# Kernel tuning notes

Hardware: AMD Instinct MI355X
Metric: run time of the kernel (lower is better)

## Reference

```python
import jax, jax.numpy as jnp
import numpy as np

B, S, T = 2, 1024, 1024          # batch, new tokens, cache length (prefill: S == T)
DIM, NH, NKV, HD = 2048, 16, 4, 128
FFN = 5632
EPS = 1e-5
STD = 0.02


def rms_norm(x, w, eps=EPS):
    return x * jax.lax.rsqrt(jnp.mean(x * x, axis=-1, keepdims=True) + eps) * w


def apply_rope(x, freqs_cis):
    # x: [B, S, H, HD]; freqs_cis: [S, HD//2, 2] (cos, sin) over consecutive pairs
    xr = x.reshape(*x.shape[:-1], HD // 2, 2)
    cos = freqs_cis[None, :, None, :, 0]
    sin = freqs_cis[None, :, None, :, 1]
    x0, x1 = xr[..., 0], xr[..., 1]
    rot = jnp.stack([x0 * cos - x1 * sin, x0 * sin + x1 * cos], axis=-1)
    return rot.reshape(x.shape)


def setup_inputs() -> dict:
    key = jax.random.key(0)
    ks = jax.random.split(key, 10)
    x = jax.random.normal(ks[0], (B, S, DIM), jnp.float32)
    # rotary tables
    inv_freq = 1.0 / (10000.0 ** (np.arange(0, HD, 2, dtype=np.float32) / HD))
    ang = np.outer(np.arange(S, dtype=np.float32), inv_freq)          # [S, HD//2]
    freqs_cis = jnp.asarray(np.stack([np.cos(ang), np.sin(ang)], -1), jnp.float32)
    cache_k = jnp.zeros((1, B, T, NKV, HD), jnp.float32)
    cache_v = jnp.zeros((1, B, T, NKV, HD), jnp.float32)
    mask = jnp.triu(jnp.full((S, T), -1e9, jnp.float32), k=1)         # additive causal
    wq = jax.random.normal(ks[1], (DIM, NH, HD), jnp.float32) * STD
    wk = jax.random.normal(ks[2], (DIM, NKV, HD), jnp.float32) * STD
    wv = jax.random.normal(ks[3], (DIM, NKV, HD), jnp.float32) * STD
    wo = jax.random.normal(ks[4], (NH * HD, DIM), jnp.float32) * STD
    w_gate = jax.random.normal(ks[5], (DIM, FFN), jnp.float32) * STD
    w_up = jax.random.normal(ks[6], (DIM, FFN), jnp.float32) * STD
    w_down = jax.random.normal(ks[7], (FFN, DIM), jnp.float32) * STD
    attn_norm_w = jnp.ones((DIM,), jnp.float32)
    ffn_norm_w = jnp.ones((DIM,), jnp.float32)
    return dict(x=x, freqs_cis=freqs_cis, cache_k=cache_k, cache_v=cache_v,
                mask=mask, wq=wq, wk=wk, wv=wv, wo=wo, w_gate=w_gate,
                w_up=w_up, w_down=w_down, attn_norm_w=attn_norm_w,
                ffn_norm_w=ffn_norm_w, layer_idx=0)


def reference(x, freqs_cis, cache_k, cache_v, mask, wq, wk, wv, wo,
              w_gate, w_up, w_down, attn_norm_w, ffn_norm_w, layer_idx):
    # --- attention sub-block ---
    h = rms_norm(x, attn_norm_w)
    q = jnp.einsum('bsd,dhk->bshk', h, wq)          # [B,S,NH,HD]
    k = jnp.einsum('bsd,dgk->bsgk', h, wk)          # [B,S,NKV,HD]
    v = jnp.einsum('bsd,dgk->bsgk', h, wv)
    q = apply_rope(q, freqs_cis)
    k = apply_rope(k, freqs_cis)
    # append to per-layer KV cache at position 0 (prefill)
    cache_k = jax.lax.dynamic_update_slice(cache_k, k[None], (layer_idx, 0, 0, 0, 0))
    cache_v = jax.lax.dynamic_update_slice(cache_v, v[None], (layer_idx, 0, 0, 0, 0))
    keys = cache_k[layer_idx]                        # [B,T,NKV,HD]
    vals = cache_v[layer_idx]
    J = NH // NKV                                    # query heads per kv head
    qg = q.reshape(B, S, NKV, J, HD)
    scale = 1.0 / jnp.sqrt(jnp.float32(HD))
    scores = jnp.einsum('bsgjd,btgd->bgjst', qg, keys) * scale  # [B,NKV,J,S,T]
    scores = scores + mask                           # broadcast [S,T]
    probs = jax.nn.softmax(scores, axis=-1)
    ctx = jnp.einsum('bgjst,btgd->bsgjd', probs, vals).reshape(B, S, NH * HD)
    x = x + ctx @ wo
    # --- SwiGLU FFN sub-block ---
    hf = rms_norm(x, ffn_norm_w)
    ffn = (jax.nn.silu(hf @ w_gate) * (hf @ w_up)) @ w_down
    x = x + ffn
    return (x, cache_k, cache_v)
```

## Files before the change

kernel.cpp:

```cpp
#include <hip/hip_runtime.h>

typedef float f32x4 __attribute__((ext_vector_type(4)));
typedef __bf16 bf16x8 __attribute__((ext_vector_type(8)));
typedef unsigned short u16;

#define DIM 2048
#define SEQ 1024
#define BSZ 2
#define NH 16
#define NKV 4
#define HD 128
#define FFNDIM 5632
#define MROWS (BSZ * SEQ)

__device__ __forceinline__ u16 f2bf(float f) {
  union { float f; unsigned u; } v; v.f = f;
  unsigned u = v.u;
  unsigned r = (u + 0x7fffu + ((u >> 16) & 1u)) >> 16;
  return (u16)r;
}
__device__ __forceinline__ float bf2f(u16 h) {
  union { unsigned u; float f; } v; v.u = ((unsigned)h) << 16; return v.f;
}

__device__ __forceinline__ void gld16(const void* g, void* l) {
  __builtin_amdgcn_global_load_lds(
      (const __attribute__((address_space(1))) unsigned int*)g,
      (__attribute__((address_space(3))) unsigned int*)l, 16, 0, 0);
}

__global__ __launch_bounds__(256) void kxpose(const float* __restrict__ W,
                                              u16* __restrict__ Wt,
                                              int K, int N, int rs, int ro) {
  __shared__ float t[64][65];
  int kb = blockIdx.y * 64, nb = blockIdx.x * 64;
  int tid = threadIdx.x;
#pragma unroll
  for (int it = 0; it < 16; ++it) {
    int idx = it * 256 + tid;
    int r = idx >> 6, c = idx & 63;
    t[r][c] = W[(size_t)(kb + r) * N + nb + c];
  }
  __syncthreads();
#pragma unroll
  for (int it = 0; it < 16; ++it) {
    int idx = it * 256 + tid;
    int rn = idx >> 6, ck = idx & 63;
    Wt[((size_t)(nb + rn) * rs + ro) * K + kb + ck] = f2bf(t[ck][rn]);
  }
}

__global__ __launch_bounds__(256) void kvxpose(const u16* __restrict__ v,
                                               u16* __restrict__ vt) {
  __shared__ u16 t[64][66];
  int bg = blockIdx.z;
  int b = bg >> 2, g = bg & 3;
  int s0 = blockIdx.x * 64, d0 = blockIdx.y * 64;
  int tid = threadIdx.x;
  int rr = tid >> 4, cc = (tid & 15) * 4;
#pragma unroll
  for (int it = 0; it < 4; ++it) {
    int r = it * 16 + rr;
    *(uint2*)&t[r][cc] =
        *(const uint2*)(v + (size_t)(b * SEQ + s0 + r) * (NKV * HD) + g * HD + d0 + cc);
  }
  __syncthreads();
#pragma unroll
  for (int it = 0; it < 4; ++it) {
    int r = it * 16 + rr;
    u16 o[4] = {t[cc][r], t[cc + 1][r], t[cc + 2][r], t[cc + 3][r]};
    *(uint2*)(vt + (size_t)((b * NKV + g) * HD + d0 + r) * SEQ + s0 + cc) = *(const uint2*)o;
  }
}

__global__ __launch_bounds__(256) void krmsnorm(const float* __restrict__ x,
                                                const float* __restrict__ w,
                                                u16* __restrict__ out) {
  int row = blockIdx.x, tid = threadIdx.x;
  const float* xr = x + (size_t)row * DIM;
  float4 a = *(const float4*)(xr + tid * 8);
  float4 b = *(const float4*)(xr + tid * 8 + 4);
  float ss = a.x * a.x + a.y * a.y + a.z * a.z + a.w * a.w +
             b.x * b.x + b.y * b.y + b.z * b.z + b.w * b.w;
#pragma unroll
  for (int off = 1; off < 64; off <<= 1) ss += __shfl_xor(ss, off, 64);
  __shared__ float red[4];
  if ((tid & 63) == 0) red[tid >> 6] = ss;
  __syncthreads();
  float tot = red[0] + red[1] + red[2] + red[3];
  float sc = rsqrtf(tot * (1.0f / DIM) + 1e-5f);
  float xs[8] = {a.x, a.y, a.z, a.w, b.x, b.y, b.z, b.w};
  const float* wr = w + tid * 8;
  u16 o[8];
#pragma unroll
  for (int j = 0; j < 8; ++j) o[j] = f2bf(xs[j] * sc * wr[j]);
  *(int4*)(out + (size_t)row * DIM + tid * 8) = *(const int4*)o;
}

__global__ __launch_bounds__(256) void krope_q(u16* __restrict__ q,
                                               const float* __restrict__ fc) {
  int t = blockIdx.x * 256 + threadIdx.x;
  int j = t & 63;
  int h = (t >> 6) & (NH - 1);
  int row = t >> 10;
  int s = row & (SEQ - 1);
  size_t off = (size_t)row * DIM + h * HD + 2 * j;
  unsigned pk = *(unsigned*)(q + off);
  float x0 = bf2f((u16)pk), x1 = bf2f((u16)(pk >> 16));
  float cs = fc[s * HD + 2 * j], sn = fc[s * HD + 2 * j + 1];
  float y0 = x0 * cs - x1 * sn;
  float y1 = x0 * sn + x1 * cs;
  *(unsigned*)(q + off) = (unsigned)f2bf(y0) | ((unsigned)f2bf(y1) << 16);
}

__global__ __launch_bounds__(256) void krope_k(u16* __restrict__ k,
                                               const float* __restrict__ fc,
                                               float* __restrict__ ck) {
  int t = blockIdx.x * 256 + threadIdx.x;
  int j = t & 63;
  int g = (t >> 6) & (NKV - 1);
  int row = t >> 8;
  int s = row & (SEQ - 1);
  size_t off = (size_t)row * (NKV * HD) + g * HD + 2 * j;
  unsigned pk = *(unsigned*)(k + off);
  float x0 = bf2f((u16)pk), x1 = bf2f((u16)(pk >> 16));
  float cs = fc[s * HD + 2 * j], sn = fc[s * HD + 2 * j + 1];
  float y0 = x0 * cs - x1 * sn;
  float y1 = x0 * sn + x1 * cs;
  *(unsigned*)(k + off) = (unsigned)f2bf(y0) | ((unsigned)f2bf(y1) << 16);
  ck[off] = y0;
  ck[off + 1] = y1;
}

template <int EPI>
__global__ __launch_bounds__(512, 4) void kgemm(
    const u16* __restrict__ A, const u16* __restrict__ Bt, int N, int K,
    u16* o0, u16* __restrict__ o1, u16* __restrict__ o2,
    float* of, const float* res) {
  __shared__ u16 As[2][128 * 64];
  __shared__ u16 Bs[2][128 * 64];
  int bn = blockIdx.x * 128, bm = blockIdx.y * 128;
  int tid = threadIdx.x, lane = tid & 63, wv = tid >> 6;
  int wm = (wv >> 2) * 64;
  int wn = (wv & 3) * 32;
  int r16 = lane & 15, grp = lane >> 4;
  int srow = lane >> 3;
  int schunk = ((lane & 7) ^ srow) * 8;
  f32x4 acc[4][2] = {};
  const u16* Abase = A + (size_t)(bm + wv * 16) * K + schunk;
  const u16* Bbase = Bt + (size_t)(bn + wv * 16) * K + schunk;
  int woff = wv * 16 * 64;

  auto STAGE = [&](int buf, int k0) {
#pragma unroll
    for (int j = 0; j < 2; ++j) {
      gld16(Abase + (size_t)(j * 8 + srow) * K + k0, &As[buf][woff + j * 512]);
      gld16(Bbase + (size_t)(j * 8 + srow) * K + k0, &Bs[buf][woff + j * 512]);
    }
  };
  auto COMPUTE = [&](int buf) {
#pragma unroll
    for (int kk = 0; kk < 2; ++kk) {
      int swz = (((kk << 2) | grp) ^ (r16 & 7)) * 8;
      bf16x8 af[4], bfr[2];
#pragma unroll
      for (int m = 0; m < 4; ++m)
        af[m] = *(const bf16x8*)&As[buf][(wm + m * 16 + r16) * 64 + swz];
#pragma unroll
      for (int n = 0; n < 2; ++n)
        bfr[n] = *(const bf16x8*)&Bs[buf][(wn + n * 16 + r16) * 64 + swz];
#pragma unroll
      for (int m = 0; m < 4; ++m)
#pragma unroll
        for (int n = 0; n < 2; ++n)
          acc[m][n] = __builtin_amdgcn_mfma_f32_16x16x32_bf16(af[m], bfr[n], acc[m][n], 0, 0, 0);
    }
  };

  STAGE(0, 0);
  int nt = K >> 6;
  for (int t = 0; t < nt; ++t) {
    int cur = t & 1;
    if (t + 1 < nt) {
      STAGE(cur ^ 1, (t + 1) << 6);
      asm volatile("s_waitcnt vmcnt(4)" ::: "memory");
    } else {
      asm volatile("s_waitcnt vmcnt(0)" ::: "memory");
    }
    __builtin_amdgcn_sched_barrier(0);
    __builtin_amdgcn_s_barrier();
    __builtin_amdgcn_sched_barrier(0);
    COMPUTE(cur);
    __builtin_amdgcn_s_barrier();
  }

#pragma unroll
  for (int mi = 0; mi < 4; ++mi) {
#pragma unroll
    for (int ni = 0; ni < 2; ++ni) {
#pragma unroll
      for (int r = 0; r < 4; ++r) {
        int gr = bm + wm + mi * 16 + grp * 4 + r;
        int gc = bn + wn + ni * 16 + r16;
        float v = acc[mi][ni][r];
        if constexpr (EPI == 0) {
          if (gc < DIM) {
            o0[(size_t)gr * DIM + gc] = f2bf(v);
          } else if (gc < DIM + 512) {
            o1[(size_t)gr * 512 + (gc - DIM)] = f2bf(v);
          } else {
            int c2 = gc - (DIM + 512);
            of[(size_t)gr * 512 + c2] = v;
            o2[(size_t)gr * 512 + c2] = f2bf(v);
          }
        } else {
          of[(size_t)gr * N + gc] = v + res[(size_t)gr * N + gc];
        }
      }
    }
  }
}

__global__ __launch_bounds__(512, 4) void kgemm_gu(
    const u16* __restrict__ A, const u16* __restrict__ Bt,
    u16* __restrict__ out) {
  const int K = DIM;
  __shared__ u16 As[2][128 * 64];
  __shared__ u16 Bs[2][128 * 64];
  int bn = blockIdx.x * 128, bm = blockIdx.y * 128;
  int tid = threadIdx.x, lane = tid & 63, wv = tid >> 6;
  int wm = (wv >> 2) * 64;
  int wn = (wv & 3) * 32;
  int r16 = lane & 15, grp = lane >> 4;
  int srow = lane >> 3;
  int schunk = ((lane & 7) ^ srow) * 8;
  f32x4 acc[4][2] = {};
  const u16* Abase = A + (size_t)(bm + wv * 16) * K + schunk;
  const u16* Bbase = Bt + (size_t)(bn + wv * 16) * K + schunk;
  int woff = wv * 16 * 64;

  auto STAGE = [&](int buf, int k0) {
#pragma unroll
    for (int j = 0; j < 2; ++j) {
      gld16(Abase + (size_t)(j * 8 + srow) * K + k0, &As[buf][woff + j * 512]);
      gld16(Bbase + (size_t)(j * 8 + srow) * K + k0, &Bs[buf][woff + j * 512]);
    }
  };
  auto COMPUTE = [&](int buf) {
#pragma unroll
    for (int kk = 0; kk < 2; ++kk) {
      int swz = (((kk << 2) | grp) ^ (r16 & 7)) * 8;
      bf16x8 af[4], bfr[2];
#pragma unroll
      for (int m = 0; m < 4; ++m)
        af[m] = *(const bf16x8*)&As[buf][(wm + m * 16 + r16) * 64 + swz];
#pragma unroll
      for (int n = 0; n < 2; ++n)
        bfr[n] = *(const bf16x8*)&Bs[buf][(wn + n * 16 + r16) * 64 + swz];
#pragma unroll
      for (int m = 0; m < 4; ++m)
#pragma unroll
        for (int n = 0; n < 2; ++n)
          acc[m][n] = __builtin_amdgcn_mfma_f32_16x16x32_bf16(af[m], bfr[n], acc[m][n], 0, 0, 0);
    }
  };

  STAGE(0, 0);
  int nt = K >> 6;
  for (int t = 0; t < nt; ++t) {
    int cur = t & 1;
    if (t + 1 < nt) {
      STAGE(cur ^ 1, (t + 1) << 6);
      asm volatile("s_waitcnt vmcnt(4)" ::: "memory");
    } else {
      asm volatile("s_waitcnt vmcnt(0)" ::: "memory");
    }
    __builtin_amdgcn_sched_barrier(0);
    __builtin_amdgcn_s_barrier();
    __builtin_amdgcn_sched_barrier(0);
    COMPUTE(cur);
    __builtin_amdgcn_s_barrier();
  }

  bool evenlane = (r16 & 1) == 0;
#pragma unroll
  for (int mi = 0; mi < 4; ++mi) {
#pragma unroll
    for (int ni = 0; ni < 2; ++ni) {
#pragma unroll
      for (int r = 0; r < 4; ++r) {
        float v = acc[mi][ni][r];
        float pv = __shfl_xor(v, 1, 64);
        if (evenlane) {
          int gr = bm + wm + mi * 16 + grp * 4 + r;
          int gc = bn + wn + ni * 16 + r16;
          float sg = v / (1.0f + __expf(-v));
          out[(size_t)gr * FFNDIM + (gc >> 1)] = f2bf(sg * pv);
        }
      }
    }
  }
}

__global__ __launch_bounds__(64) void kattn(const u16* __restrict__ qb,
                                            const u16* __restrict__ kb,
                                            const u16* __restrict__ vtb,
                                            u16* __restrict__ ctxb) {
  __shared__ u16 Plds[16][72];
  int l = threadIdx.x;
  int qt = gridDim.x - 1 - blockIdx.x;
  int h = blockIdx.y, b = blockIdx.z;
  int g = h >> 2;
  int q0 = qt * 16;
  int r16 = l & 15, grp = l >> 4;
  const float scale = 0.08838834764831845f;
  bf16x8 qf[4];
  {
    const u16* qrow = qb + (size_t)(b * SEQ + q0 + r16) * DIM + h * HD + grp * 8;
#pragma unroll
    for (int c = 0; c < 4; ++c) qf[c] = *(const bf16x8*)(qrow + c * 32);
  }
  const u16* vt = vtb + (size_t)(b * NKV + g) * HD * SEQ;
  f32x4 ctx[8] = {};
  float m = -1e30f, lsum = 0.0f;
  int q_idx = q0 + r16;
  int ttmax = (q0 + 15) >> 6;
  for (int tt = 0; tt <= ttmax; ++tt) {
    int t0 = tt * 64;
    f32x4 d[4] = {{0.f, 0.f, 0.f, 0.f}, {0.f, 0.f, 0.f, 0.f},
                  {0.f, 0.f, 0.f, 0.f}, {0.f, 0.f, 0.f, 0.f}};
    const u16* kbase = kb + (size_t)(b * SEQ + t0 + r16) * (NKV * HD) + g * HD + grp * 8;
    __builtin_amdgcn_s_setprio(1);
#pragma unroll
    for (int c = 0; c < 4; ++c) {
#pragma unroll
      for (int ch = 0; ch < 4; ++ch) {
        bf16x8 kf = *(const bf16x8*)(kbase + (size_t)(ch * 16) * (NKV * HD) + c * 32);
        d[ch] = __builtin_amdgcn_mfma_f32_16x16x32_bf16(kf, qf[c], d[ch], 0, 0, 0);
      }
    }
    __builtin_amdgcn_s_setprio(0);
    float p[16];
    float mx = -1e30f;
#pragma unroll
    for (int ch = 0; ch < 4; ++ch) {
#pragma unroll
      for (int r = 0; r < 4; ++r) {
        int tA = t0 + ch * 16 + grp * 4 + r;
        float s = d[ch][r] * scale;
        if (tA > q_idx) s = -1e30f;
        p[ch * 4 + r] = s;
        mx = fmaxf(mx, s);
      }
    }
    mx = fmaxf(mx, __shfl_xor(mx, 16, 64));
    mx = fmaxf(mx, __shfl_xor(mx, 32, 64));
    if (!__all(mx - m <= 8.0f)) {
      float mnew = fmaxf(m, mx);
      float corr = __expf(m - mnew);
      lsum *= corr;
      float cf[4];
#pragma unroll
      for (int r = 0; r < 4; ++r) cf[r] = __shfl(corr, grp * 4 + r, 64);
#pragma unroll
      for (int dc = 0; dc < 8; ++dc)
#pragma unroll
        for (int r = 0; r < 4; ++r) ctx[dc][r] *= cf[r];
      m = mnew;
    }
    float psum = 0.f;
#pragma unroll
    for (int i = 0; i < 16; ++i) {
      p[i] = __expf(p[i] - m);
      psum += p[i];
    }
    psum += __shfl_xor(psum, 16, 64);
    psum += __shfl_xor(psum, 32, 64);
    lsum += psum;
#pragma unroll
    for (int ch = 0; ch < 4; ++ch) {
      unsigned w0 = (unsigned)f2bf(p[ch * 4]) | ((unsigned)f2bf(p[ch * 4 + 1]) << 16);
      unsigned w1 = (unsigned)f2bf(p[ch * 4 + 2]) | ((unsigned)f2bf(p[ch * 4 + 3]) << 16);
      *(unsigned*)&Plds[r16][ch * 16 + grp * 4] = w0;
      *(unsigned*)&Plds[r16][ch * 16 + grp * 4 + 2] = w1;
    }
    bf16x8 pa0, pa1;
    {
      union { bf16x8 v; int4 q; } u0, u1;
      u0.q = *(const int4*)&Plds[r16][grp * 8];
      u1.q = *(const int4*)&Plds[r16][32 + grp * 8];
      pa0 = u0.v;
      pa1 = u1.v;
    }
    __builtin_amdgcn_s_setprio(1);
#pragma unroll
    for (int dc = 0; dc < 8; ++dc) {
      bf16x8 vf0 = *(const bf16x8*)(vt + (size_t)(dc * 16 + r16) * SEQ + t0 + grp * 8);
      bf16x8 vf1 = *(const bf16x8*)(vt + (size_t)(dc * 16 + r16) * SEQ + t0 + 32 + grp * 8);
      ctx[dc] = __builtin_amdgcn_mfma_f32_16x16x32_bf16(pa0, vf0, ctx[dc], 0, 0, 0);
      ctx[dc] = __builtin_amdgcn_mfma_f32_16x16x32_bf16(pa1, vf1, ctx[dc], 0, 0, 0);
    }
    __builtin_amdgcn_s_setprio(0);
  }
  float linv = 1.0f / lsum;
  float lf[4];
#pragma unroll
  for (int r = 0; r < 4; ++r) lf[r] = __shfl(linv, grp * 4 + r, 64);
  u16* crow = ctxb + (size_t)(b * SEQ + q0) * DIM + h * HD;
#pragma unroll
  for (int dc = 0; dc < 8; ++dc)
#pragma unroll
    for (int r = 0; r < 4; ++r)
      crow[(size_t)(grp * 4 + r) * DIM + dc * 16 + r16] = f2bf(ctx[dc][r] * lf[r]);
}

extern "C" void kernel_launch(void* const* d_in, const int* in_sizes, int n_in,
                              void* d_out, int out_size, void* d_ws, size_t ws_size,
                              hipStream_t stream) {
  const float* x = (const float*)d_in[0];
  const float* fc = (const float*)d_in[1];
  const float* wq = (const float*)d_in[5];
  const float* wk = (const float*)d_in[6];
  const float* wv = (const float*)d_in[7];
  const float* wo = (const float*)d_in[8];
  const float* wg = (const float*)d_in[9];
  const float* wu = (const float*)d_in[10];
  const float* wd = (const float*)d_in[11];
  const float* anw = (const float*)d_in[12];
  const float* fnw = (const float*)d_in[13];

  float* out_x = (float*)d_out;
  float* out_ck = out_x + (size_t)MROWS * DIM;
  float* out_cv = out_ck + (size_t)MROWS * NKV * HD;

  char* ws = (char*)d_ws;
  u16* h_b    = (u16*)(ws);
  u16* q_b    = (u16*)(ws + (8u << 20));
  u16* k_b    = (u16*)(ws + (16u << 20));
  u16* v_b    = (u16*)(ws + (18u << 20));
  u16* ctx_b  = (u16*)(ws + (20u << 20));
  u16* hf_b   = (u16*)(ws + (28u << 20));
  u16* Wt     = (u16*)(ws + (60u << 20));
  u16* vt_b   = h_b;
  u16* Wt_gu  = (u16*)(ws + (36u << 20));
  u16* g_b    = (u16*)(ws);
  u16* Wt_dn  = (u16*)(ws + (36u << 20));

  kxpose<<<dim3(2048 / 64, 2048 / 64), 256, 0, stream>>>(wq, Wt, 2048, 2048, 1, 0);
  kxpose<<<dim3(512 / 64, 2048 / 64), 256, 0, stream>>>(wk, Wt + (size_t)2048 * 2048, 2048, 512, 1, 0);
  kxpose<<<dim3(512 / 64, 2048 / 64), 256, 0, stream>>>(wv, Wt + (size_t)2560 * 2048, 2048, 512, 1, 0);

  krmsnorm<<<MROWS, 256, 0, stream>>>(x, anw, h_b);
  kgemm<0><<<dim3(3072 / 128, 16), 512, 0, stream>>>(h_b, Wt, 3072, 2048,
                                                     q_b, k_b, v_b, out_cv, nullptr);
  krope_q<<<8192, 256, 0, stream>>>(q_b, fc);
  krope_k<<<2048, 256, 0, stream>>>(k_b, fc, out_ck);
  kvxpose<<<dim3(SEQ / 64, HD / 64, BSZ * NKV), 256, 0, stream>>>(v_b, vt_b);
  kattn<<<dim3(SEQ / 16, NH, BSZ), 64, 0, stream>>>(q_b, k_b, vt_b, ctx_b);

  kxpose<<<dim3(32, 32), 256, 0, stream>>>(wo, Wt, 2048, 2048, 1, 0);
  kgemm<2><<<dim3(16, 16), 512, 0, stream>>>(ctx_b, Wt, 2048, 2048,
                                             nullptr, nullptr, nullptr, out_x, x);
  krmsnorm<<<MROWS, 256, 0, stream>>>(out_x, fnw, hf_b);

  kxpose<<<dim3(5632 / 64, 2048 / 64), 256, 0, stream>>>(wg, Wt_gu, 2048, 5632, 2, 0);
  kxpose<<<dim3(5632 / 64, 2048 / 64), 256, 0, stream>>>(wu, Wt_gu, 2048, 5632, 2, 1);
  kgemm_gu<<<dim3(11264 / 128, 16), 512, 0, stream>>>(hf_b, Wt_gu, g_b);
  kxpose<<<dim3(2048 / 64, 5632 / 64), 256, 0, stream>>>(wd, Wt_dn, 5632, 2048, 1, 0);
  kgemm<2><<<dim3(16, 16), 512, 0, stream>>>(g_b, Wt_dn, 2048, 5632,
                                             nullptr, nullptr, nullptr, out_x, out_x);
}
```

Baseline: 462.9 us.

## Split causal attention over key chunks with a separate softmax combine kernel

The attention kernel now splits each query tile's key range into up to four 256-key chunks, one block per chunk. Each block writes an unnormalized fp32 partial context plus its running max and sum to workspace, and a new combine kernel merges them with log-sum-exp weighting into the bf16 context. This shortens the longest per-block loop and evens out the causal load imbalance across the grid. The cost is extra global traffic for the fp32 partials, one more kernel launch, and many blocks that exit immediately.

```diff
diff --git a/kernel.cpp b/kernel.cpp
--- a/kernel.cpp
+++ b/kernel.cpp
@@ -305,11 +305,15 @@
 __global__ __launch_bounds__(64) void kattn(const u16* __restrict__ qb,
                                             const u16* __restrict__ kb,
                                             const u16* __restrict__ vtb,
-                                            u16* __restrict__ ctxb) {
+                                            float* __restrict__ part_c,
+                                            float* __restrict__ part_ml) {
   __shared__ u16 Plds[16][72];
   int l = threadIdx.x;
-  int qt = gridDim.x - 1 - blockIdx.x;
-  int h = blockIdx.y, b = blockIdx.z;
+  int qt = blockIdx.x, h = blockIdx.y;
+  int bz = blockIdx.z;
+  int b = bz >> 2, chunk = bz & 3;
+  int gi = qt >> 4;
+  if (chunk > gi) return;
   int g = h >> 2;
   int q0 = qt * 16;
   int r16 = l & 15, grp = l >> 4;
@@ -324,9 +328,9 @@
   f32x4 ctx[8] = {};
   float m = -1e30f, lsum = 0.0f;
   int q_idx = q0 + r16;
-  int ttmax = (q0 + 15) >> 6;
-  for (int tt = 0; tt <= ttmax; ++tt) {
-    int t0 = tt * 64;
+  int tstart = chunk * 256;
+  int tend = min(tstart + 256, q0 + 16);
+  for (int t0 = tstart; t0 < tend; t0 += 64) {
     f32x4 d[4] = {{0.f, 0.f, 0.f, 0.f}, {0.f, 0.f, 0.f, 0.f},
                   {0.f, 0.f, 0.f, 0.f}, {0.f, 0.f, 0.f, 0.f}};
     const u16* kbase = kb + (size_t)(b * SEQ + t0 + r16) * (NKV * HD) + g * HD + grp * 8;
@@ -402,16 +406,50 @@
     }
     __builtin_amdgcn_s_setprio(0);
   }
-  float linv = 1.0f / lsum;
-  float lf[4];
-#pragma unroll
-  for (int r = 0; r < 4; ++r) lf[r] = __shfl(linv, grp * 4 + r, 64);
-  u16* crow = ctxb + (size_t)(b * SEQ + q0) * DIM + h * HD;
+  int widx = (b * NH + h) * 160 + 8 * gi * (gi + 1) + (qt & 15) * (gi + 1) + chunk;
+  float* dst = part_c + (size_t)widx * 2048;
 #pragma unroll
   for (int dc = 0; dc < 8; ++dc)
 #pragma unroll
     for (int r = 0; r < 4; ++r)
-      crow[(size_t)(grp * 4 + r) * DIM + dc * 16 + r16] = f2bf(ctx[dc][r] * lf[r]);
+      dst[(grp * 4 + r) * 128 + dc * 16 + r16] = ctx[dc][r];
+  if (l < 16) {
+    part_ml[(size_t)widx * 32 + l] = m;
+    part_ml[(size_t)widx * 32 + 16 + l] = lsum;
+  }
+}
+
+__global__ __launch_bounds__(256) void kcombine(const float* __restrict__ part_c,
+                                                const float* __restrict__ part_ml,
+                                                u16* __restrict__ ctxb) {
+  int idx = blockIdx.x;
+  int qt = idx & 63;
+  int h = (idx >> 6) & 15;
+  int b = idx >> 10;
+  int gi = qt >> 4;
+  int nch = gi + 1;
+  int base = (b * NH + h) * 160 + 8 * gi * (gi + 1) + (qt & 15) * nch;
+  int t = threadIdx.x;
+  int row = t >> 4, c0 = (t & 15) * 8;
+  float M = -1e30f;
+  for (int i = 0; i < nch; ++i)
+    M = fmaxf(M, part_ml[(size_t)(base + i) * 32 + row]);
+  float L = 0.f;
+  float o[8] = {};
+  for (int i = 0; i < nch; ++i) {
+    float mi = part_ml[(size_t)(base + i) * 32 + row];
+    float li = part_ml[(size_t)(base + i) * 32 + 16 + row];
+    float w = __expf(mi - M);
+    L += w * li;
+    const float* p = part_c + (size_t)(base + i) * 2048 + row * 128 + c0;
+#pragma unroll
+    for (int j = 0; j < 8; ++j) o[j] += w * p[j];
+  }
+  float inv = 1.0f / L;
+  u16 ob[8];
+#pragma unroll
+  for (int j = 0; j < 8; ++j) ob[j] = f2bf(o[j] * inv);
+  *(int4*)(ctxb + (size_t)(b * SEQ + qt * 16 + row) * DIM + h * HD + c0) = *(const int4*)ob;
 }
 
 extern "C" void kernel_launch(void* const* d_in, const int* in_sizes, int n_in,
@@ -445,6 +483,8 @@
   u16* Wt_gu  = (u16*)(ws + (36u << 20));
   u16* g_b    = (u16*)(ws);
   u16* Wt_dn  = (u16*)(ws + (36u << 20));
+  float* part_c  = (float*)(ws + (28u << 20));
+  float* part_ml = (float*)(ws + (68u << 20));
 
   kxpose<<<dim3(2048 / 64, 2048 / 64), 256, 0, stream>>>(wq, Wt, 2048, 2048, 1, 0);
   kxpose<<<dim3(512 / 64, 2048 / 64), 256, 0, stream>>>(wk, Wt + (size_t)2048 * 2048, 2048, 512, 1, 0);
@@ -456,7 +496,8 @@
   krope_q<<<8192, 256, 0, stream>>>(q_b, fc);
   krope_k<<<2048, 256, 0, stream>>>(k_b, fc, out_ck);
   kvxpose<<<dim3(SEQ / 64, HD / 64, BSZ * NKV), 256, 0, stream>>>(v_b, vt_b);
-  kattn<<<dim3(SEQ / 16, NH, BSZ), 64, 0, stream>>>(q_b, k_b, vt_b, ctx_b);
+  kattn<<<dim3(SEQ / 16, NH, BSZ * 4), 64, 0, stream>>>(q_b, k_b, vt_b, part_c, part_ml);
+  kcombine<<<BSZ * NH * (SEQ / 16), 256, 0, stream>>>(part_c, part_ml, ctx_b);
 
   kxpose<<<dim3(32, 32), 256, 0, stream>>>(wo, Wt, 2048, 2048, 1, 0);
   kgemm<2><<<dim3(16, 16), 512, 0, stream>>>(ctx_b, Wt, 2048, 2048,
```

Measured after the change: 451.8 us. 2.4% less time.

## Stage K/V tiles in LDS with double-buffered async loads across four waves

Applied to the files above, without the earlier changes.

The attention kernel now runs four waves per block, each handling 16 query rows of a 64-row query block. K and V^T tiles are loaded cooperatively into swizzled, double-buffered shared memory via async global-to-LDS loads, with the next tile prefetched while the current one is computed. The aim is to stop each wave from re-reading the same K/V from global memory and to overlap those loads with MFMA work. In exchange the kernel adds barriers, uses more LDS (which may limit occupancy), and the causal tile bound is now taken per block rather than per wave.

```diff
diff --git a/kernel.cpp b/kernel.cpp
--- a/kernel.cpp
+++ b/kernel.cpp
@@ -302,16 +302,19 @@
   }
 }
 
-__global__ __launch_bounds__(64) void kattn(const u16* __restrict__ qb,
-                                            const u16* __restrict__ kb,
-                                            const u16* __restrict__ vtb,
-                                            u16* __restrict__ ctxb) {
-  __shared__ u16 Plds[16][72];
-  int l = threadIdx.x;
-  int qt = gridDim.x - 1 - blockIdx.x;
+__global__ __launch_bounds__(256) void kattn(const u16* __restrict__ qb,
+                                             const u16* __restrict__ kb,
+                                             const u16* __restrict__ vtb,
+                                             u16* __restrict__ ctxb) {
+  __shared__ u16 Ks[2][64 * 128];
+  __shared__ u16 Vs[2][128 * 64];
+  __shared__ u16 Plds[4][16][72];
+  int tid = threadIdx.x;
+  int l = tid & 63, wv = tid >> 6;
+  int qg = 15 - blockIdx.x;
   int h = blockIdx.y, b = blockIdx.z;
   int g = h >> 2;
-  int q0 = qt * 16;
+  int q0 = qg * 64 + wv * 16;
   int r16 = l & 15, grp = l >> 4;
   const float scale = 0.08838834764831845f;
   bf16x8 qf[4];
@@ -320,22 +323,53 @@
 #pragma unroll
     for (int c = 0; c < 4; ++c) qf[c] = *(const bf16x8*)(qrow + c * 32);
   }
-  const u16* vt = vtb + (size_t)(b * NKV + g) * HD * SEQ;
+  const u16* kg = kb + (size_t)b * SEQ * (NKV * HD) + g * HD;
+  const u16* vg = vtb + (size_t)((b * NKV + g) * HD) * SEQ;
+
+  auto STAGE = [&](int buf, int t0) {
+#pragma unroll
+    for (int p = 0; p < 4; ++p) {
+      int row = p * 16 + wv * 4 + (l >> 4);
+      int ch = (l & 15) ^ (row & 7);
+      gld16(kg + (size_t)(t0 + row) * (NKV * HD) + ch * 8,
+            &Ks[buf][p * 2048 + wv * 512]);
+    }
+#pragma unroll
+    for (int p = 0; p < 4; ++p) {
+      int row = p * 32 + wv * 8 + (l >> 3);
+      int ch = (l & 7) ^ (row & 7);
+      gld16(vg + (size_t)row * SEQ + t0 + ch * 8,
+            &Vs[buf][p * 2048 + wv * 512]);
+    }
+  };
+
   f32x4 ctx[8] = {};
   float m = -1e30f, lsum = 0.0f;
   int q_idx = q0 + r16;
-  int ttmax = (q0 + 15) >> 6;
-  for (int tt = 0; tt <= ttmax; ++tt) {
+  int ntiles = qg + 1;
+
+  STAGE(0, 0);
+  for (int tt = 0; tt < ntiles; ++tt) {
+    int cur = tt & 1;
+    if (tt + 1 < ntiles) {
+      STAGE(cur ^ 1, (tt + 1) * 64);
+      asm volatile("s_waitcnt vmcnt(8)" ::: "memory");
+    } else {
+      asm volatile("s_waitcnt vmcnt(0)" ::: "memory");
+    }
+    __builtin_amdgcn_sched_barrier(0);
+    __builtin_amdgcn_s_barrier();
+    __builtin_amdgcn_sched_barrier(0);
     int t0 = tt * 64;
     f32x4 d[4] = {{0.f, 0.f, 0.f, 0.f}, {0.f, 0.f, 0.f, 0.f},
                   {0.f, 0.f, 0.f, 0.f}, {0.f, 0.f, 0.f, 0.f}};
-    const u16* kbase = kb + (size_t)(b * SEQ + t0 + r16) * (NKV * HD) + g * HD + grp * 8;
     __builtin_amdgcn_s_setprio(1);
 #pragma unroll
     for (int c = 0; c < 4; ++c) {
 #pragma unroll
       for (int ch = 0; ch < 4; ++ch) {
-        bf16x8 kf = *(const bf16x8*)(kbase + (size_t)(ch * 16) * (NKV * HD) + c * 32);
+        int row = ch * 16 + r16;
+        bf16x8 kf = *(const bf16x8*)&Ks[cur][row * 128 + (((c * 4 + grp) ^ (row & 7)) * 8)];
         d[ch] = __builtin_amdgcn_mfma_f32_16x16x32_bf16(kf, qf[c], d[ch], 0, 0, 0);
       }
     }
@@ -381,26 +415,28 @@
     for (int ch = 0; ch < 4; ++ch) {
       unsigned w0 = (unsigned)f2bf(p[ch * 4]) | ((unsigned)f2bf(p[ch * 4 + 1]) << 16);
       unsigned w1 = (unsigned)f2bf(p[ch * 4 + 2]) | ((unsigned)f2bf(p[ch * 4 + 3]) << 16);
-      *(unsigned*)&Plds[r16][ch * 16 + grp * 4] = w0;
-      *(unsigned*)&Plds[r16][ch * 16 + grp * 4 + 2] = w1;
+      *(unsigned*)&Plds[wv][r16][ch * 16 + grp * 4] = w0;
+      *(unsigned*)&Plds[wv][r16][ch * 16 + grp * 4 + 2] = w1;
     }
     bf16x8 pa0, pa1;
     {
       union { bf16x8 v; int4 q; } u0, u1;
-      u0.q = *(const int4*)&Plds[r16][grp * 8];
-      u1.q = *(const int4*)&Plds[r16][32 + grp * 8];
+      u0.q = *(const int4*)&Plds[wv][r16][grp * 8];
+      u1.q = *(const int4*)&Plds[wv][r16][32 + grp * 8];
       pa0 = u0.v;
       pa1 = u1.v;
     }
     __builtin_amdgcn_s_setprio(1);
 #pragma unroll
     for (int dc = 0; dc < 8; ++dc) {
-      bf16x8 vf0 = *(const bf16x8*)(vt + (size_t)(dc * 16 + r16) * SEQ + t0 + grp * 8);
-      bf16x8 vf1 = *(const bf16x8*)(vt + (size_t)(dc * 16 + r16) * SEQ + t0 + 32 + grp * 8);
+      int row = dc * 16 + r16;
+      bf16x8 vf0 = *(const bf16x8*)&Vs[cur][row * 64 + ((grp ^ (row & 7)) * 8)];
+      bf16x8 vf1 = *(const bf16x8*)&Vs[cur][row * 64 + (((grp + 4) ^ (row & 7)) * 8)];
       ctx[dc] = __builtin_amdgcn_mfma_f32_16x16x32_bf16(pa0, vf0, ctx[dc], 0, 0, 0);
       ctx[dc] = __builtin_amdgcn_mfma_f32_16x16x32_bf16(pa1, vf1, ctx[dc], 0, 0, 0);
     }
     __builtin_amdgcn_s_setprio(0);
+    __builtin_amdgcn_s_barrier();
   }
   float linv = 1.0f / lsum;
   float lf[4];
@@ -456,7 +492,7 @@
   krope_q<<<8192, 256, 0, stream>>>(q_b, fc);
   krope_k<<<2048, 256, 0, stream>>>(k_b, fc, out_ck);
   kvxpose<<<dim3(SEQ / 64, HD / 64, BSZ * NKV), 256, 0, stream>>>(v_b, vt_b);
-  kattn<<<dim3(SEQ / 16, NH, BSZ), 64, 0, stream>>>(q_b, k_b, vt_b, ctx_b);
+  kattn<<<dim3(SEQ / 64, NH, BSZ), 256, 0, stream>>>(q_b, k_b, vt_b, ctx_b);
 
   kxpose<<<dim3(32, 32), 256, 0, stream>>>(wo, Wt, 2048, 2048, 1, 0);
   kgemm<2><<<dim3(16, 16), 512, 0, stream>>>(ctx_b, Wt, 2048, 2048,
```

Result: faster. 387.0 us (-16.4%).
